# Kernel tuning notes

Hardware: AMD Instinct MI355X
Metric: run time of the kernel (lower is better)

The kernel has to match this reference:

```python
import jax, jax.numpy as jnp
import numpy as np

N, E = 50000, 800000
F_IN, F_OUT, H = 128, 16, 8
NEG_SLOPE = 0.2  # PyG GATConv default
EPS = 1e-5       # LayerNorm eps


def setup_inputs() -> dict:
    key = jax.random.key(0)
    ks = jax.random.split(key, 8)
    x = jax.random.normal(ks[0], (N, F_IN), dtype=jnp.float32)
    edge_index = jax.random.randint(ks[1], (2, E), 0, N, dtype=jnp.int32)
    s_in = 1.0 / np.sqrt(F_IN)
    s_f = 1.0 / np.sqrt(F_OUT)
    W = jax.random.normal(ks[2], (F_IN, H * F_OUT), dtype=jnp.float32) * s_in
    att_src = jax.random.normal(ks[3], (H, F_OUT), dtype=jnp.float32) * s_f
    att_dst = jax.random.normal(ks[4], (H, F_OUT), dtype=jnp.float32) * s_f
    bias = jnp.zeros((H * F_OUT,), dtype=jnp.float32)
    gamma = jnp.ones((H * F_OUT,), dtype=jnp.float32)
    beta = jnp.zeros((H * F_OUT,), dtype=jnp.float32)
    return {"x": x, "edge_index": edge_index, "W": W, "att_src": att_src,
            "att_dst": att_dst, "bias": bias, "gamma": gamma, "beta": beta}


def _gat_layer(x, edge_index, W, att_src, att_dst, bias, gamma, beta):
    n = x.shape[0]
    # add self loops (PyG GATConv default add_self_loops=True)
    loop = jnp.arange(n, dtype=edge_index.dtype)
    src = jnp.concatenate([edge_index[0], loop])  # message source j
    dst = jnp.concatenate([edge_index[1], loop])  # message target i

    xp = (x @ W).reshape(n, H, F_OUT)                      # [N,H,F]
    a_src = jnp.einsum('nhf,hf->nh', xp, att_src)          # [N,H]
    a_dst = jnp.einsum('nhf,hf->nh', xp, att_dst)          # [N,H]

    e = a_src[src] + a_dst[dst]                            # [E+N,H]
    e = jax.nn.leaky_relu(e, NEG_SLOPE)
    # softmax over incoming edges per destination node
    m = jax.ops.segment_max(e, dst, num_segments=n)        # [N,H]
    e = jnp.exp(e - m[dst])
    z = jax.ops.segment_sum(e, dst, num_segments=n)        # [N,H]
    alpha = e / jnp.where(z[dst] > 0, z[dst], 1.0)         # [E+N,H]

    msg = alpha[:, :, None] * xp[src]                      # [E+N,H,F]
    out = jax.ops.segment_sum(msg, dst, num_segments=n)    # [N,H,F]
    out = out.reshape(n, H * F_OUT) + bias

    # LayerNorm over feature dim
    mu = out.mean(axis=-1, keepdims=True)
    var = out.var(axis=-1, keepdims=True)
    return (out - mu) * jax.lax.rsqrt(var + EPS) * gamma + beta


def reference(x, edge_index, W, att_src, att_dst, bias, gamma, beta):
    return _gat_layer(x, edge_index, W, att_src, att_dst, bias, gamma, beta)
```

## Files before the change

kernel.cpp:

```cpp
#include <hip/hip_runtime.h>
#include <math.h>

#define F_IN 128
#define NHD 8
#define FEAT 128
#define NEG_SLOPE 0.2f
#define LN_EPS 1e-5f
#define BSH 7
#define BMSK 127
#define NPQ 16
#define CAP 48
#define EPB 2048
#define NBMAX 512
#define BCAP 6144
#define WCOLS 144

typedef __bf16 v8bf __attribute__((ext_vector_type(8)));
typedef __bf16 v2bf __attribute__((ext_vector_type(2)));
typedef float f32x4 __attribute__((ext_vector_type(4)));

__global__ __launch_bounds__(256) void k_wt(const float* __restrict__ W,
                                            const float* __restrict__ att_src,
                                            const float* __restrict__ att_dst,
                                            __bf16* __restrict__ WT) {
    int idx = blockIdx.x * 256 + threadIdx.x;
    int c = idx >> 7, k = idx & 127;
    float v;
    if (c < 128) {
        v = W[k * 128 + c];
    } else if (c < 136) {
        int h = c - 128;
        float s = 0.f;
#pragma unroll
        for (int f = 0; f < 16; ++f) s += W[k * 128 + h * 16 + f] * att_src[h * 16 + f];
        v = s;
    } else {
        int h = c - 136;
        float s = 0.f;
#pragma unroll
        for (int f = 0; f < 16; ++f) s += W[k * 128 + h * 16 + f] * att_dst[h * 16 + f];
        v = s;
    }
    WT[c * 128 + k] = (__bf16)v;
}

__global__ __launch_bounds__(512) void k_fused(const float* __restrict__ x,
                                               const __bf16* __restrict__ WT,
                                               __bf16* __restrict__ xp16,
                                               float* __restrict__ a_src,
                                               float* __restrict__ a_dst,
                                               const int* __restrict__ src,
                                               const int* __restrict__ dst,
                                               unsigned int* __restrict__ sorted_g,
                                               int* __restrict__ runptr,
                                               int n, int E, int Ga) {
    __shared__ __bf16 xs[64][136];
    if ((int)blockIdx.x < Ga) {
        __shared__ int lcnt[NBMAX];
        __shared__ int loff[NBMAX + 1];
        __shared__ unsigned int sorted_l[EPB];
        __shared__ int wtot[8], wexcl[8];
        int NB = (n + BMSK) >> BSH;
        int tid = threadIdx.x, lane = tid & 63, wid = tid >> 6;
        long base0 = (long)blockIdx.x * EPB;
        long total = (long)E + n;
        if (tid < NB) lcnt[tid] = 0;
        __syncthreads();

        int s0[4], d0[4];
        bool val[4];
        long e0 = base0 + (long)tid * 4;
        if (e0 + 3 < E) {
            int4 sv = *(const int4*)(src + e0);
            int4 dv = *(const int4*)(dst + e0);
            s0[0] = sv.x; s0[1] = sv.y; s0[2] = sv.z; s0[3] = sv.w;
            d0[0] = dv.x; d0[1] = dv.y; d0[2] = dv.z; d0[3] = dv.w;
            val[0] = val[1] = val[2] = val[3] = true;
        } else {
#pragma unroll
            for (int j = 0; j < 4; ++j) {
                long e = e0 + j;
                val[j] = (e < total);
                s0[j] = d0[j] = 0;
                if (val[j]) {
                    if (e < E) { s0[j] = src[e]; d0[j] = dst[e]; }
                    else { s0[j] = d0[j] = (int)(e - E); }
                }
            }
        }
#pragma unroll
        for (int j = 0; j < 4; ++j)
            if (val[j]) atomicAdd(&lcnt[d0[j] >> BSH], 1);
        __syncthreads();

        int v = (tid < NB) ? lcnt[tid] : 0;
        int xx = v;
#pragma unroll
        for (int o = 1; o < 64; o <<= 1) {
            int t2 = __shfl_up(xx, o);
            if (lane >= o) xx += t2;
        }
        if (lane == 63) wtot[wid] = xx;
        __syncthreads();
        if (wid == 0 && lane < 8) {
            int s = wtot[lane];
            int y = s;
#pragma unroll
            for (int o = 1; o < 8; o <<= 1) {
                int t2 = __shfl_up(y, o);
                if (lane >= o) y += t2;
            }
            wexcl[lane] = y - s;
        }
        __syncthreads();
        int excl = wexcl[wid] + xx - v;
        if (tid < NB) loff[tid] = excl;
        if (tid == NB - 1) loff[NB] = excl + v;
        __syncthreads();
        if (tid < NB) lcnt[tid] = loff[tid];
        __syncthreads();
#pragma unroll
        for (int j = 0; j < 4; ++j) {
            if (val[j]) {
                int b = d0[j] >> BSH;
                int pos = atomicAdd(&lcnt[b], 1);
                sorted_l[pos] = ((unsigned)s0[j] << BSH) | (unsigned)(d0[j] & BMSK);
            }
        }
        __syncthreads();
        int tv = loff[NB];
        for (int i = tid; i < tv; i += 512)
            sorted_g[base0 + i] = sorted_l[i];
        if (tid <= NB) runptr[(long)blockIdx.x * (NBMAX + 1) + tid] = loff[tid];
    } else {
        int gb = blockIdx.x - Ga;
        int tid = threadIdx.x;
        int rowbase = gb * 64;
        {
            int i4 = tid;
#pragma unroll
            for (int rep = 0; rep < 4; ++rep, i4 += 512) {
                int r = i4 >> 5, c4 = i4 & 31;
                int gr = rowbase + r; if (gr > n - 1) gr = n - 1;
                float4 xv = *(const float4*)(x + (long)gr * 128 + c4 * 4);
                __bf16* p = &xs[r][c4 * 4];
                p[0] = (__bf16)xv.x; p[1] = (__bf16)xv.y;
                p[2] = (__bf16)xv.z; p[3] = (__bf16)xv.w;
            }
        }
        __syncthreads();
        int wv = tid >> 6;
        int lane = tid & 63;
        int m = lane & 15, quad = lane >> 4;
        int colbase = wv * 16;
        const __bf16* wcol = WT + (colbase + m) * 128;
        v8bf wf[4];
#pragma unroll
        for (int kk = 0; kk < 4; ++kk)
            wf[kk] = *(const v8bf*)(wcol + kk * 32 + quad * 8);
        v8bf wf2[4];
        if (wv < 4) {
            const __bf16* wcol2 = WT + (128 + m) * 128;
#pragma unroll
            for (int kk = 0; kk < 4; ++kk)
                wf2[kk] = *(const v8bf*)(wcol2 + kk * 32 + quad * 8);
        }
#pragma unroll
        for (int t = 0; t < 4; ++t) {
            int rb = t * 16;
            f32x4 acc = {0.f, 0.f, 0.f, 0.f};
#pragma unroll
            for (int kk = 0; kk < 4; ++kk) {
                v8bf a = *(const v8bf*)(&xs[rb + m][kk * 32 + quad * 8]);
                acc = __builtin_amdgcn_mfma_f32_16x16x32_bf16(a, wf[kk], acc, 0, 0, 0);
            }
#pragma unroll
            for (int r = 0; r < 4; ++r) {
                int row = rowbase + rb + quad * 4 + r;
                if (row < n)
                    xp16[(long)row * 128 + colbase + m] = (__bf16)acc[r];
            }
        }
        if (wv < 4) {
            int rb = wv * 16;
            f32x4 acc = {0.f, 0.f, 0.f, 0.f};
#pragma unroll
            for (int kk = 0; kk < 4; ++kk) {
                v8bf a = *(const v8bf*)(&xs[rb + m][kk * 32 + quad * 8]);
                acc = __builtin_amdgcn_mfma_f32_16x16x32_bf16(a, wf2[kk], acc, 0, 0, 0);
            }
#pragma unroll
            for (int r = 0; r < 4; ++r) {
                int row = rowbase + rb + quad * 4 + r;
                if (row < n) {
                    if (m < 8) a_src[row * 8 + m] = acc[r];
                    else       a_dst[row * 8 + (m - 8)] = acc[r];
                }
            }
        }
    }
}

__global__ __launch_bounds__(256) void k_reorder(const unsigned int* __restrict__ sorted_g,
                                                 const int* __restrict__ runptr,
                                                 unsigned int* __restrict__ sorted2,
                                                 int* __restrict__ bcnt, int Ga) {
    int b = blockIdx.x;
    int tid = threadIdx.x, lane = tid & 63, wid = tid >> 6;
    __shared__ int wsum[4], wexcl_s[4];
    __shared__ int carry_s;
    if (tid == 0) carry_s = 0;
    __syncthreads();
    for (int base = 0; base < Ga; base += 256) {
        int blk = base + tid;
        int st = 0, c = 0;
        if (blk < Ga) {
            const int* rp = runptr + (long)blk * (NBMAX + 1) + b;
            st = rp[0];
            c = rp[1] - st;
        }
        int xx = c;
#pragma unroll
        for (int o = 1; o < 64; o <<= 1) {
            int t2 = __shfl_up(xx, o);
            if (lane >= o) xx += t2;
        }
        if (lane == 63) wsum[wid] = xx;
        __syncthreads();
        if (tid == 0) {
            int s = 0;
#pragma unroll
            for (int w = 0; w < 4; ++w) { wexcl_s[w] = s; s += wsum[w]; }
            wsum[0] = s;
        }
        __syncthreads();
        int excl = carry_s + wexcl_s[wid] + xx - c;
        const unsigned int* sg = sorted_g + (long)blk * EPB + st;
        unsigned int* dp = sorted2 + (long)b * BCAP + excl;
        int lim = BCAP - excl;
        for (int i = 0; i < c && i < lim; ++i) dp[i] = sg[i];
        __syncthreads();
        if (tid == 0) carry_s += wsum[0];
        __syncthreads();
    }
    if (tid == 0) bcnt[b] = carry_s < BCAP ? carry_s : BCAP;
}

__global__ __launch_bounds__(256) void k_ba(const unsigned int* __restrict__ sorted2,
                                            const int* __restrict__ bcnt,
                                            const float* __restrict__ a_src,
                                            const float* __restrict__ a_dst,
                                            const __bf16* __restrict__ xp16,
                                            const float* __restrict__ bias,
                                            const float* __restrict__ gamma,
                                            const float* __restrict__ beta,
                                            const int* __restrict__ src,
                                            const int* __restrict__ dst,
                                            float* __restrict__ out, int n, int E) {
    __shared__ int slds[NPQ * CAP];
    __shared__ int lc[NPQ];
    __shared__ float adst_s[NPQ * NHD];
    int b = blockIdx.x >> 3;
    int q = blockIdx.x & 7;
    int tid = threadIdx.x;
    int node0 = (b << BSH) + q * NPQ;
    if (tid < NPQ) lc[tid] = 0;
    if (tid < NPQ * NHD) {
        int nd = node0 + (tid >> 3);
        adst_s[tid] = (nd < n) ? a_dst[nd * NHD + (tid & 7)] : 0.f;
    }
    __syncthreads();

    int cnt_b = bcnt[b];
    const unsigned int* sg = sorted2 + (long)b * BCAP;
    int qlo = q * NPQ;
    for (int i = tid; i < cnt_b; i += 256) {
        unsigned int u = sg[i];
        int dl = (int)(u & BMSK) - qlo;
        if ((unsigned)dl < (unsigned)NPQ) {
            int p = atomicAdd(&lc[dl], 1);
            if (p < CAP) slds[dl * CAP + p] = (int)(u >> BSH);
        }
    }
    __syncthreads();
    if (tid < NPQ) {
        int cc = lc[tid]; if (cc > CAP) cc = CAP;
        int pad = (cc + 7) & ~7; if (pad > CAP) pad = CAP;
        for (int p = cc; p < pad; ++p) slds[tid * CAP + p] = 0;
    }
    __syncthreads();

    int lane = tid & 63, wv = tid >> 6;
    int h = lane & 7, j8 = lane >> 3;
    float2 bs = *(const float2*)(bias + 2 * lane);
    float2 g  = *(const float2*)(gamma + 2 * lane);
    float2 bt = *(const float2*)(beta + 2 * lane);

    for (int i = wv; i < NPQ; i += 4) {
        int node = node0 + i;
        if (node >= n) break;
        int cnt = lc[i];
        float acc0 = 0.f, acc1 = 0.f, inv;

        if (cnt <= CAP) {
            const int* row = slds + i * CAP;
            float b_h = adst_s[i * NHD + h];
            float zacc = 0.f;
            for (int base = 0; base < cnt; base += 8) {
                int s_my = row[base + j8];
                float e = a_src[s_my * NHD + h] + b_h;
                e = e > 0.f ? e : NEG_SLOPE * e;
                float w_my = (base + j8 < cnt) ? __expf(e) : 0.f;
                zacc += w_my;
                int ss[8];
#pragma unroll
                for (int j = 0; j < 8; ++j) ss[j] = row[base + j];
                float2 vals[8];
#pragma unroll
                for (int j = 0; j < 8; ++j) {
                    v2bf p = *(const v2bf*)(xp16 + (long)ss[j] * FEAT + 2 * lane);
                    vals[j] = make_float2((float)p[0], (float)p[1]);
                }
#pragma unroll
                for (int j = 0; j < 8; ++j) {
                    float w = __shfl(w_my, j * 8 + j8);
                    acc0 = fmaf(w, vals[j].x, acc0);
                    acc1 = fmaf(w, vals[j].y, acc1);
                }
            }
            zacc += __shfl_xor(zacc, 8);
            zacc += __shfl_xor(zacc, 16);
            zacc += __shfl_xor(zacc, 32);
            float z = __shfl(zacc, j8);
            inv = 1.f / z;
        } else {
            float b_h = a_dst[node * NHD + j8];
            float z = 0.f;
            {
                float e = a_src[node * NHD + j8] + b_h;
                e = e > 0.f ? e : NEG_SLOPE * e;
                float w = __expf(e);
                z += w;
                v2bf p = *(const v2bf*)(xp16 + (long)node * FEAT + 2 * lane);
                acc0 = fmaf(w, (float)p[0], acc0);
                acc1 = fmaf(w, (float)p[1], acc1);
            }
            for (int base = 0; base < E; base += 64) {
                int e = base + lane;
                int sv = 0;
                bool mt = false;
                if (e < E) { mt = (dst[e] == node); if (mt) sv = src[e]; }
                unsigned long long mask = __ballot(mt);
                while (mask) {
                    int bl = __ffsll(mask) - 1;
                    mask &= mask - 1;
                    int s = __shfl(sv, bl);
                    float ee = a_src[s * NHD + j8] + b_h;
                    ee = ee > 0.f ? ee : NEG_SLOPE * ee;
                    float w = __expf(ee);
                    z += w;
                    v2bf p = *(const v2bf*)(xp16 + (long)s * FEAT + 2 * lane);
                    acc0 = fmaf(w, (float)p[0], acc0);
                    acc1 = fmaf(w, (float)p[1], acc1);
                }
            }
            inv = 1.f / z;
        }

        float v0 = acc0 * inv + bs.x;
        float v1 = acc1 * inv + bs.y;
        float ssum = v0 + v1;
        float ssq = v0 * v0 + v1 * v1;
#pragma unroll
        for (int o = 32; o > 0; o >>= 1) {
            ssum += __shfl_xor(ssum, o);
            ssq += __shfl_xor(ssq, o);
        }
        float mu = ssum * (1.0f / FEAT);
        float var = ssq * (1.0f / FEAT) - mu * mu;
        float rs = rsqrtf(var + LN_EPS);
        float2 o2;
        o2.x = (v0 - mu) * rs * g.x + bt.x;
        o2.y = (v1 - mu) * rs * g.y + bt.y;
        *(float2*)(out + (long)node * FEAT + 2 * lane) = o2;
    }
}

extern "C" void kernel_launch(void* const* d_in, const int* in_sizes, int n_in,
                              void* d_out, int out_size, void* d_ws, size_t ws_size,
                              hipStream_t stream) {
    const float* x = (const float*)d_in[0];
    const int* edge_index = (const int*)d_in[1];
    const float* W = (const float*)d_in[2];
    const float* att_src = (const float*)d_in[3];
    const float* att_dst = (const float*)d_in[4];
    const float* bias = (const float*)d_in[5];
    const float* gamma = (const float*)d_in[6];
    const float* beta = (const float*)d_in[7];
    float* out = (float*)d_out;

    int n = in_sizes[0] / F_IN;
    int E = in_sizes[1] / 2;
    const int* src = edge_index;
    const int* dst = edge_index + E;
    int NB = (n + BMSK) >> BSH;
    int Ga = (E + n + EPB - 1) / EPB;
    int Gg = (n + 63) / 64;

    char* ws = (char*)d_ws;
    __bf16* WT   = (__bf16*)ws;                    ws += (size_t)WCOLS * 128 * 2;
    __bf16* xp16 = (__bf16*)ws;                    ws += (size_t)n * FEAT * 2;
    float* a_src = (float*)ws;                     ws += (size_t)n * NHD * 4;
    float* a_dst = (float*)ws;                     ws += (size_t)n * NHD * 4;
    unsigned int* sorted_g = (unsigned int*)ws;    ws += (size_t)Ga * EPB * 4;
    unsigned int* sorted2 = (unsigned int*)ws;     ws += (size_t)NB * BCAP * 4;
    int* bcnt = (int*)ws;                          ws += (size_t)NB * 4;
    int* runptr  = (int*)ws;                       ws += (size_t)Ga * (NBMAX + 1) * 4;

    k_wt<<<72, 256, 0, stream>>>(W, att_src, att_dst, WT);
    k_fused<<<Ga + Gg, 512, 0, stream>>>(x, WT, xp16, a_src, a_dst,
                                         src, dst, sorted_g, runptr, n, E, Ga);
    k_reorder<<<NB, 256, 0, stream>>>(sorted_g, runptr, sorted2, bcnt, Ga);
    k_ba<<<NB * 8, 256, 0, stream>>>(sorted2, bcnt, a_src, a_dst, xp16,
                                     bias, gamma, beta, src, dst, out, n, E);
}
```

Measured before the change: 165.5 us.

## Scatter edge buckets directly via global atomics, drop reorder kernel, stage xp16 stores

Each partition block now reserves space in the per-bucket destination array with a global atomicAdd on a bucket counter and writes its locally sorted edges straight into place. This removes the intermediate sorted_g/runptr buffers and the separate k_reorder kernel with its serial per-thread copy loops. The GEMM path also stages its bf16 outputs in shared memory so xp16 is written with coalesced 16-byte row stores. The trade-off is that edge order inside each bucket is now nondeterministic and the global atomics can contend.

```diff
diff --git a/kernel.cpp b/kernel.cpp
--- a/kernel.cpp
+++ b/kernel.cpp
@@ -22,8 +22,10 @@
 __global__ __launch_bounds__(256) void k_wt(const float* __restrict__ W,
                                             const float* __restrict__ att_src,
                                             const float* __restrict__ att_dst,
-                                            __bf16* __restrict__ WT) {
+                                            __bf16* __restrict__ WT,
+                                            int* __restrict__ gcnt, int NB) {
     int idx = blockIdx.x * 256 + threadIdx.x;
+    if (idx < NB) gcnt[idx] = 0;
     int c = idx >> 7, k = idx & 127;
     float v;
     if (c < 128) {
@@ -51,15 +53,17 @@
                                                float* __restrict__ a_dst,
                                                const int* __restrict__ src,
                                                const int* __restrict__ dst,
-                                               unsigned int* __restrict__ sorted_g,
-                                               int* __restrict__ runptr,
+                                               unsigned int* __restrict__ sorted2,
+                                               int* __restrict__ gcnt,
                                                int n, int E, int Ga) {
-    __shared__ __bf16 xs[64][136];
+    __shared__ __align__(16) char smem[34816];
     if ((int)blockIdx.x < Ga) {
-        __shared__ int lcnt[NBMAX];
-        __shared__ int loff[NBMAX + 1];
-        __shared__ unsigned int sorted_l[EPB];
-        __shared__ int wtot[8], wexcl[8];
+        unsigned int* sorted_l = (unsigned int*)smem;
+        int* lcnt = (int*)(smem + 8192);
+        int* loff = (int*)(smem + 8192 + 2048);
+        int* wtot = (int*)(smem + 8192 + 2048 + 2052);
+        int* wexcl = (int*)(smem + 8192 + 2048 + 2052 + 32);
+        int* goff = (int*)(smem + 8192 + 2048 + 2052 + 64);
         int NB = (n + BMSK) >> BSH;
         int tid = threadIdx.x, lane = tid & 63, wid = tid >> 6;
         long base0 = (long)blockIdx.x * EPB;
@@ -124,15 +128,27 @@
             if (val[j]) {
                 int b = d0[j] >> BSH;
                 int pos = atomicAdd(&lcnt[b], 1);
-                sorted_l[pos] = ((unsigned)s0[j] << BSH) | (unsigned)(d0[j] & BMSK);
-            }
+                sorted_l[pos] = ((unsigned)b << 23) | ((unsigned)s0[j] << 7) |
+                                (unsigned)(d0[j] & BMSK);
+            }
+        }
+        __syncthreads();
+        if (tid < NB) {
+            int len = loff[tid + 1] - loff[tid];
+            goff[tid] = (len > 0) ? atomicAdd(&gcnt[tid], len) : 0;
         }
         __syncthreads();
         int tv = loff[NB];
-        for (int i = tid; i < tv; i += 512)
-            sorted_g[base0 + i] = sorted_l[i];
-        if (tid <= NB) runptr[(long)blockIdx.x * (NBMAX + 1) + tid] = loff[tid];
+        for (int i = tid; i < tv; i += 512) {
+            unsigned int u = sorted_l[i];
+            int b = (int)(u >> 23);
+            int r = goff[b] + (i - loff[b]);
+            if (r < BCAP)
+                sorted2[(long)b * BCAP + r] = u & 0x7FFFFFu;
+        }
     } else {
+        __bf16 (*xs)[136] = (__bf16 (*)[136])smem;
+        __bf16 (*ot)[136] = (__bf16 (*)[136])(smem + 17408);
         int gb = blockIdx.x - Ga;
         int tid = threadIdx.x;
         int rowbase = gb * 64;
@@ -175,11 +191,8 @@
                 acc = __builtin_amdgcn_mfma_f32_16x16x32_bf16(a, wf[kk], acc, 0, 0, 0);
             }
 #pragma unroll
-            for (int r = 0; r < 4; ++r) {
-                int row = rowbase + rb + quad * 4 + r;
-                if (row < n)
-                    xp16[(long)row * 128 + colbase + m] = (__bf16)acc[r];
-            }
+            for (int r = 0; r < 4; ++r)
+                ot[rb + quad * 4 + r][colbase + m] = (__bf16)acc[r];
         }
         if (wv < 4) {
             int rb = wv * 16;
@@ -198,52 +211,18 @@
                 }
             }
         }
-    }
-}
-
-__global__ __launch_bounds__(256) void k_reorder(const unsigned int* __restrict__ sorted_g,
-                                                 const int* __restrict__ runptr,
-                                                 unsigned int* __restrict__ sorted2,
-                                                 int* __restrict__ bcnt, int Ga) {
-    int b = blockIdx.x;
-    int tid = threadIdx.x, lane = tid & 63, wid = tid >> 6;
-    __shared__ int wsum[4], wexcl_s[4];
-    __shared__ int carry_s;
-    if (tid == 0) carry_s = 0;
-    __syncthreads();
-    for (int base = 0; base < Ga; base += 256) {
-        int blk = base + tid;
-        int st = 0, c = 0;
-        if (blk < Ga) {
-            const int* rp = runptr + (long)blk * (NBMAX + 1) + b;
-            st = rp[0];
-            c = rp[1] - st;
-        }
-        int xx = c;
-#pragma unroll
-        for (int o = 1; o < 64; o <<= 1) {
-            int t2 = __shfl_up(xx, o);
-            if (lane >= o) xx += t2;
-        }
-        if (lane == 63) wsum[wid] = xx;
-        __syncthreads();
-        if (tid == 0) {
-            int s = 0;
-#pragma unroll
-            for (int w = 0; w < 4; ++w) { wexcl_s[w] = s; s += wsum[w]; }
-            wsum[0] = s;
-        }
-        __syncthreads();
-        int excl = carry_s + wexcl_s[wid] + xx - c;
-        const unsigned int* sg = sorted_g + (long)blk * EPB + st;
-        unsigned int* dp = sorted2 + (long)b * BCAP + excl;
-        int lim = BCAP - excl;
-        for (int i = 0; i < c && i < lim; ++i) dp[i] = sg[i];
-        __syncthreads();
-        if (tid == 0) carry_s += wsum[0];
-        __syncthreads();
-    }
-    if (tid == 0) bcnt[b] = carry_s < BCAP ? carry_s : BCAP;
+        __syncthreads();
+        int r0 = tid >> 4, c8 = tid & 15;
+#pragma unroll
+        for (int pass = 0; pass < 2; ++pass) {
+            int r = r0 + pass * 32;
+            int gr = rowbase + r;
+            if (gr < n) {
+                v8bf vv = *(const v8bf*)(&ot[r][c8 * 8]);
+                *(v8bf*)(xp16 + (long)gr * FEAT + c8 * 8) = vv;
+            }
+        }
+    }
 }
 
 __global__ __launch_bounds__(256) void k_ba(const unsigned int* __restrict__ sorted2,
@@ -271,7 +250,7 @@
     }
     __syncthreads();
 
-    int cnt_b = bcnt[b];
+    int cnt_b = bcnt[b]; if (cnt_b > BCAP) cnt_b = BCAP;
     const unsigned int* sg = sorted2 + (long)b * BCAP;
     int qlo = q * NPQ;
     for (int i = tid; i < cnt_b; i += 256) {
@@ -412,15 +391,12 @@
     __bf16* xp16 = (__bf16*)ws;                    ws += (size_t)n * FEAT * 2;
     float* a_src = (float*)ws;                     ws += (size_t)n * NHD * 4;
     float* a_dst = (float*)ws;                     ws += (size_t)n * NHD * 4;
-    unsigned int* sorted_g = (unsigned int*)ws;    ws += (size_t)Ga * EPB * 4;
     unsigned int* sorted2 = (unsigned int*)ws;     ws += (size_t)NB * BCAP * 4;
-    int* bcnt = (int*)ws;                          ws += (size_t)NB * 4;
-    int* runptr  = (int*)ws;                       ws += (size_t)Ga * (NBMAX + 1) * 4;
-
-    k_wt<<<72, 256, 0, stream>>>(W, att_src, att_dst, WT);
+    int* gcnt = (int*)ws;                          ws += (size_t)NB * 4;
+
+    k_wt<<<72, 256, 0, stream>>>(W, att_src, att_dst, WT, gcnt, NB);
     k_fused<<<Ga + Gg, 512, 0, stream>>>(x, WT, xp16, a_src, a_dst,
-                                         src, dst, sorted_g, runptr, n, E, Ga);
-    k_reorder<<<NB, 256, 0, stream>>>(sorted_g, runptr, sorted2, bcnt, Ga);
-    k_ba<<<NB * 8, 256, 0, stream>>>(sorted2, bcnt, a_src, a_dst, xp16,
+                                         src, dst, sorted2, gcnt, n, E, Ga);
+    k_ba<<<NB * 8, 256, 0, stream>>>(sorted2, gcnt, a_src, a_dst, xp16,
                                      bias, gamma, beta, src, dst, out, n, E);
 }
```

Result: faster. 153.1 us (-7.5%).
